# Kernel tuning notes

Measured on AMD Instinct MI355X. Metric: run time of the kernel, lower is better.

Reference implementation:

```python
import jax, jax.numpy as jnp
import numpy as np

H = 256  # hidden_size


def setup_inputs() -> dict:
    key = jax.random.key(0)
    ks = jax.random.split(key, 9)
    std = 1.0 / np.sqrt(H)
    u = lambda k, shape: jax.random.uniform(k, shape, jnp.float32, -std, std)
    x = jax.random.normal(ks[0], (64, 16, 128, 64), jnp.float32)
    return {
        "x": x,
        "wi0": u(ks[1], (64, 3 * H)),
        "wh0": u(ks[2], (H, 3 * H)),
        "bi0": u(ks[3], (3 * H,)),
        "bh0": u(ks[4], (3 * H,)),
        "wi1": u(ks[5], (H, 3 * H)),
        "wh1": u(ks[6], (H, 3 * H)),
        "bi1": u(ks[7], (3 * H,)),
        "bh1": u(ks[8], (3 * H,)),
    }


def _cell(x_t, h, wi, wh, bi, bh):
    # x_t: (B, N, D), h: (B, N, H). Gates concatenated as [r|z|n].
    gi = x_t @ wi + bi           # (B, N, 3H)
    gh = h @ wh + bh             # (B, N, 3H)
    ir, iz, inn = jnp.split(gi, 3, axis=-1)
    hr, hz, hn = jnp.split(gh, 3, axis=-1)
    r = jax.nn.sigmoid(ir + hr)
    z = jax.nn.sigmoid(iz + hz)
    n = jnp.tanh(inn + r * hn)
    return (1.0 - z) * n + z * h


def reference(x, wi0, wh0, bi0, bh0, wi1, wh1, bi1, bh1):
    seq_len, B, N, _ = x.shape
    h0 = jnp.zeros((B, N, H), x.dtype)
    h1 = jnp.zeros((B, N, H), x.dtype)

    def step(carry, x_t):
        h0, h1 = carry
        h0 = _cell(x_t, h0, wi0, wh0, bi0, bh0)
        h1 = _cell(h0, h1, wi1, wh1, bi1, bh1)
        return (h0, h1), h1

    (h0, h1), output = jax.lax.scan(step, (h0, h1), x)
    hidden_out = jnp.stack([h0, h1], axis=0)  # (num_layers, B, N, H)
    return output, hidden_out
```

## Files before the change

### kernel.cpp

```cpp
#include <hip/hip_runtime.h>


typedef __attribute__((ext_vector_type(8))) __bf16 bf8;
typedef __attribute__((ext_vector_type(8))) unsigned short u16x8;
typedef __attribute__((ext_vector_type(4))) float f32x4;

#define MFMA16(A, B, C) __builtin_amdgcn_mfma_f32_16x16x32_bf16((A), (B), (C), 0, 0, 0)

#define ROWS 2048
#define HID 256
#define NW 768
#define SLOT (ROWS * HID)
#define OUT_HID_OFF ((size_t)64 * ROWS * HID)
#define R0SLOT 524288

static __device__ __forceinline__ float b2f(unsigned short u) {
  union { unsigned u32; float f; } v;
  v.u32 = ((unsigned)u) << 16;
  return v.f;
}
static __device__ __forceinline__ unsigned short f2b(float f) {
  unsigned u = __float_as_uint(f);
  u += 0x7fffu + ((u >> 16) & 1u);
  return (unsigned short)(u >> 16);
}
static __device__ __forceinline__ float sigm(float x) {
  return 1.0f / (1.0f + __expf(-x));
}
static __device__ __forceinline__ float tanh_fast(float x) {
  x = fminf(15.0f, fmaxf(-15.0f, x));
  float e = __expf(2.0f * x);
  return (e - 1.0f) / (e + 1.0f);
}
static __device__ __forceinline__ float ldin(const void* p, int i, int f32w) {
  return f32w ? ((const float*)p)[i] : b2f(((const unsigned short*)p)[i]);
}
static __device__ __forceinline__ void stout(void* p, size_t i, float v, int f32w) {
  if (f32w) ((float*)p)[i] = v;
  else ((unsigned short*)p)[i] = f2b(v);
}

static __device__ __forceinline__ u16x8 ld_h16(const unsigned short* p) {
  union { unsigned long long q[2]; u16x8 b; } u;
  u.q[0] = __hip_atomic_load((const unsigned long long*)p, __ATOMIC_RELAXED,
                             __HIP_MEMORY_SCOPE_AGENT);
  u.q[1] = __hip_atomic_load((const unsigned long long*)(p + 4), __ATOMIC_RELAXED,
                             __HIP_MEMORY_SCOPE_AGENT);
  return u.b;
}
static __device__ __forceinline__ void st_h16(unsigned short* p, u16x8 v) {
  union { u16x8 s; unsigned long long q[2]; } u;
  u.s = v;
  __hip_atomic_store((unsigned long long*)p, u.q[0], __ATOMIC_RELAXED,
                     __HIP_MEMORY_SCOPE_AGENT);
  __hip_atomic_store((unsigned long long*)(p + 4), u.q[1], __ATOMIC_RELAXED,
                     __HIP_MEMORY_SCOPE_AGENT);
}

__global__ void probe_dtype(const unsigned short* x, unsigned* flag) {
  if (blockIdx.x != 0 || threadIdx.x != 0) return;
  int cnt = 0;
  for (int i = 0; i < 256; ++i) {
    float v = b2f(x[i]);
    if (v == v && fabsf(v) <= 8.0f) cnt++;
  }
  *flag = (cnt >= 250) ? 0u : 1u;
}

__global__ void pack_w(const void* __restrict__ W,
                       unsigned short* __restrict__ P, int KK,
                       const unsigned* __restrict__ flag) {
  int i = blockIdx.x * blockDim.x + threadIdx.x;
  int total = 48 * KK * 64;
  if (i >= total) return;
  int f32w = (int)*flag;
  int l = i & 63;
  int kk = (i >> 6) % KK;
  int nb = i / (64 * KK);
  int n = nb * 16 + (l & 15);
  int k0 = kk * 32 + (l >> 4) * 8;
  u16x8 tmp;
#pragma unroll
  for (int e = 0; e < 8; ++e) tmp[e] = f2b(ldin(W, (k0 + e) * NW + n, f32w));
  *(u16x8*)(P + (size_t)i * 8) = tmp;
}

__global__ void __launch_bounds__(256, 1) gru_main(
    const void* __restrict__ x,
    const void* __restrict__ bi0, const void* __restrict__ bh0,
    const void* __restrict__ bi1, const void* __restrict__ bh1,
    const unsigned short* __restrict__ pwi0, const unsigned short* __restrict__ pwh0,
    const unsigned short* __restrict__ pwi1, const unsigned short* __restrict__ pwh1,
    void* __restrict__ out,
    unsigned short* __restrict__ ring0, unsigned short* __restrict__ ring1,
    unsigned* __restrict__ flags, const unsigned* __restrict__ flag) {
  __shared__ __align__(16) unsigned short AS[16384];
  __shared__ __align__(16) unsigned short HS[2][2304];

  const int f32w = (int)*flag;
  const int tid = threadIdx.x;
  const int lane = tid & 63;
  const int wid = tid >> 6;
  const int bid = blockIdx.x;
  const int g = bid >> 2;
  const int slice = bid & 3;
  const int nb = slice * 4 + wid;

  const int d = nb * 16 + (lane & 15);
  const int rb = g * 32;
  const int arow = rb + (lane & 15);
  const int koff = (lane >> 4) * 8;
  const int rl = (lane >> 4) * 4;
  const int cl = wid * 16 + (lane & 15);

  unsigned* flagp = flags + (size_t)g * 64;

  const unsigned short* xw  = pwi0 + (size_t)nb * 1024;
  const unsigned short* w0  = pwh0 + (size_t)nb * 4096;
  const unsigned short* w1i = pwi1 + (size_t)nb * 4096;
  const unsigned short* w1h = pwh1 + (size_t)nb * 4096;

  const float iR0 = ldin(bi0, d, f32w) + ldin(bh0, d, f32w);
  const float iZ0 = ldin(bi0, 256 + d, f32w) + ldin(bh0, 256 + d, f32w);
  const float iI0 = ldin(bi0, 512 + d, f32w);
  const float iH0 = ldin(bh0, 512 + d, f32w);
  const float iR1 = ldin(bi1, d, f32w) + ldin(bh1, d, f32w);
  const float iZ1 = ldin(bi1, 256 + d, f32w) + ldin(bh1, 256 + d, f32w);
  const float iI1 = ldin(bi1, 512 + d, f32w);
  const float iH1 = ldin(bh1, 512 + d, f32w);

  float h0p[2][4] = {{0, 0, 0, 0}, {0, 0, 0, 0}};
  float h1p[2][4] = {{0, 0, 0, 0}, {0, 0, 0, 0}};

  const int ef = tid >> 7;
  const int ekk = (tid >> 6) & 1;
  const int eln = tid & 63;
  const int ehs = (ef * 16 + (eln & 15)) * 72 + ekk * 32 + (eln >> 4) * 8;
  const size_t ero = (size_t)g * 8192 +
                     (size_t)(ef * 8 + slice * 2 + ekk) * 512 + eln * 8;

  for (int t = 0; t <= 64; ++t) {
    const int sc = t & 1;
    const int sp = sc ^ 1;

    f32x4 aR0[2], aZ0[2], aI0[2], aH0[2], aR1[2], aZ1[2], aI1[2], aH1[2];
#pragma unroll
    for (int f = 0; f < 2; ++f) {
      aR0[f] = (f32x4){iR0, iR0, iR0, iR0};
      aZ0[f] = (f32x4){iZ0, iZ0, iZ0, iZ0};
      aI0[f] = (f32x4){iI0, iI0, iI0, iI0};
      aH0[f] = (f32x4){iH0, iH0, iH0, iH0};
      aR1[f] = (f32x4){iR1, iR1, iR1, iR1};
      aZ1[f] = (f32x4){iZ1, iZ1, iZ1, iZ1};
      aI1[f] = (f32x4){iI1, iI1, iI1, iI1};
      aH1[f] = (f32x4){iH1, iH1, iH1, iH1};
    }

    if (t < 64) {
      size_t xoff = ((size_t)t * ROWS + arow) * 64 + koff;
#pragma unroll
      for (int kk = 0; kk < 2; ++kk) {
        union { u16x8 u; bf8 b; } A0, A1;
        if (f32w) {
          const float* ab = (const float*)x + xoff;
#pragma unroll
          for (int e = 0; e < 8; ++e) {
            A0.u[e] = f2b(ab[kk * 32 + e]);
            A1.u[e] = f2b(ab[16 * 64 + kk * 32 + e]);
          }
        } else {
          const unsigned short* ab = (const unsigned short*)x + xoff;
          A0.u = *(const u16x8*)(ab + kk * 32);
          A1.u = *(const u16x8*)(ab + 16 * 64 + kk * 32);
        }
        const int lb = lane * 8;
        bf8 Br = *(const bf8*)(xw + 0 * 16384 + kk * 512 + lb);
        bf8 Bz = *(const bf8*)(xw + 1 * 16384 + kk * 512 + lb);
        bf8 Bn = *(const bf8*)(xw + 2 * 16384 + kk * 512 + lb);
        aR0[0] = MFMA16(A0.b, Br, aR0[0]);
        aR0[1] = MFMA16(A1.b, Br, aR0[1]);
        aZ0[0] = MFMA16(A0.b, Bz, aZ0[0]);
        aZ0[1] = MFMA16(A1.b, Bz, aZ0[1]);
        aI0[0] = MFMA16(A0.b, Bn, aI0[0]);
        aI0[1] = MFMA16(A1.b, Bn, aI0[1]);
      }
    }

    if (t > 0 && tid == 0) {
      const unsigned tgt = 4u * (unsigned)t;
      while (__hip_atomic_load(flagp, __ATOMIC_RELAXED,
                               __HIP_MEMORY_SCOPE_AGENT) < tgt)
        __builtin_amdgcn_s_sleep(1);
    }
    __syncthreads();

    {
      const unsigned short* r0 = ring0 + (size_t)sp * R0SLOT + (size_t)g * 8192;
#pragma unroll
      for (int i = 0; i < 4; ++i) {
        int idx = tid + i * 256;
        int ff = idx >> 6, ln2 = idx & 63;
        *(u16x8*)(AS + ff * 512 + ln2 * 8) = ld_h16(r0 + ff * 512 + ln2 * 8);
      }
      if (t >= 2) {
        const unsigned short* r1 = ring1 + (size_t)sc * R0SLOT + (size_t)g * 8192;
#pragma unroll
        for (int i = 0; i < 4; ++i) {
          int idx = tid + i * 256;
          int ff = idx >> 6, ln2 = idx & 63;
          *(u16x8*)(AS + 8192 + ff * 512 + ln2 * 8) =
              ld_h16(r1 + ff * 512 + ln2 * 8);
        }
      }
    }
    __syncthreads();

#pragma unroll
    for (int kk = 0; kk < 8; ++kk) {
      const int lb = lane * 8;
      bf8 A0 = *(const bf8*)(AS + (0 * 8 + kk) * 512 + lb);
      bf8 A1 = *(const bf8*)(AS + (1 * 8 + kk) * 512 + lb);
      bf8 Br0 = *(const bf8*)(w0 + 0 * 65536 + kk * 512 + lb);
      bf8 Bz0 = *(const bf8*)(w0 + 1 * 65536 + kk * 512 + lb);
      bf8 Bn0 = *(const bf8*)(w0 + 2 * 65536 + kk * 512 + lb);
      bf8 Br1 = *(const bf8*)(w1i + 0 * 65536 + kk * 512 + lb);
      bf8 Bz1 = *(const bf8*)(w1i + 1 * 65536 + kk * 512 + lb);
      bf8 Bn1 = *(const bf8*)(w1i + 2 * 65536 + kk * 512 + lb);
      aR0[0] = MFMA16(A0, Br0, aR0[0]);
      aR0[1] = MFMA16(A1, Br0, aR0[1]);
      aZ0[0] = MFMA16(A0, Bz0, aZ0[0]);
      aZ0[1] = MFMA16(A1, Bz0, aZ0[1]);
      aH0[0] = MFMA16(A0, Bn0, aH0[0]);
      aH0[1] = MFMA16(A1, Bn0, aH0[1]);
      aR1[0] = MFMA16(A0, Br1, aR1[0]);
      aR1[1] = MFMA16(A1, Br1, aR1[1]);
      aZ1[0] = MFMA16(A0, Bz1, aZ1[0]);
      aZ1[1] = MFMA16(A1, Bz1, aZ1[1]);
      aI1[0] = MFMA16(A0, Bn1, aI1[0]);
      aI1[1] = MFMA16(A1, Bn1, aI1[1]);
    }
    if (t >= 2) {
#pragma unroll
      for (int kk = 0; kk < 8; ++kk) {
        const int lb = lane * 8;
        bf8 A0 = *(const bf8*)(AS + 8192 + (0 * 8 + kk) * 512 + lb);
        bf8 A1 = *(const bf8*)(AS + 8192 + (1 * 8 + kk) * 512 + lb);
        bf8 Br = *(const bf8*)(w1h + 0 * 65536 + kk * 512 + lb);
        bf8 Bz = *(const bf8*)(w1h + 1 * 65536 + kk * 512 + lb);
        bf8 Bn = *(const bf8*)(w1h + 2 * 65536 + kk * 512 + lb);
        aR1[0] = MFMA16(A0, Br, aR1[0]);
        aR1[1] = MFMA16(A1, Br, aR1[1]);
        aZ1[0] = MFMA16(A0, Bz, aZ1[0]);
        aZ1[1] = MFMA16(A1, Bz, aZ1[1]);
        aH1[0] = MFMA16(A0, Bn, aH1[0]);
        aH1[1] = MFMA16(A1, Bn, aH1[1]);
      }
    }

    if (t < 64) {
#pragma unroll
      for (int f = 0; f < 2; ++f) {
#pragma unroll
        for (int j = 0; j < 4; ++j) {
          float r = sigm(aR0[f][j]);
          float z = sigm(aZ0[f][j]);
          float n = tanh_fast(aI0[f][j] + r * aH0[f][j]);
          float hv = (1.0f - z) * n + z * h0p[f][j];
          h0p[f][j] = hv;
          HS[0][(f * 16 + rl + j) * 72 + cl] = f2b(hv);
        }
      }
    }
    if (t >= 1) {
#pragma unroll
      for (int f = 0; f < 2; ++f) {
#pragma unroll
        for (int j = 0; j < 4; ++j) {
          float r = sigm(aR1[f][j]);
          float z = sigm(aZ1[f][j]);
          float n = tanh_fast(aI1[f][j] + r * aH1[f][j]);
          float hv = (1.0f - z) * n + z * h1p[f][j];
          h1p[f][j] = hv;
          HS[1][(f * 16 + rl + j) * 72 + cl] = f2b(hv);
        }
      }
    }
    __syncthreads();

    if (t < 64) {
      st_h16(ring0 + (size_t)sc * R0SLOT + ero, *(const u16x8*)(&HS[0][ehs]));
      if (t >= 1)
        st_h16(ring1 + (size_t)sp * R0SLOT + ero, *(const u16x8*)(&HS[1][ehs]));
    }

    asm volatile("s_waitcnt vmcnt(0)" ::: "memory");
    __syncthreads();
    if (t < 64 && tid == 0)
      __hip_atomic_fetch_add(flagp, 1u, __ATOMIC_RELAXED,
                             __HIP_MEMORY_SCOPE_AGENT);

    if (t >= 1) {
      const int tm1 = t - 1;
#pragma unroll
      for (int f = 0; f < 2; ++f) {
#pragma unroll
        for (int j = 0; j < 4; ++j) {
          int row = rb + f * 16 + rl + j;
          stout(out, ((size_t)tm1 * ROWS + row) * HID + d, h1p[f][j], f32w);
          if (tm1 == 63)
            stout(out, OUT_HID_OFF + (size_t)SLOT + (size_t)row * HID + d,
                  h1p[f][j], f32w);
        }
      }
    }
    if (t == 63) {
#pragma unroll
      for (int f = 0; f < 2; ++f) {
#pragma unroll
        for (int j = 0; j < 4; ++j) {
          int row = rb + f * 16 + rl + j;
          stout(out, OUT_HID_OFF + (size_t)row * HID + d, h0p[f][j], f32w);
        }
      }
    }
  }
}

extern "C" void kernel_launch(void* const* d_in, const int* in_sizes, int n_in,
                              void* d_out, int out_size, void* d_ws, size_t ws_size,
                              hipStream_t stream) {
  (void)in_sizes; (void)n_in; (void)out_size; (void)ws_size;
  const void* x   = d_in[0];
  const void* wi0 = d_in[1];
  const void* wh0 = d_in[2];
  const void* bi0 = d_in[3];
  const void* bh0 = d_in[4];
  const void* wi1 = d_in[5];
  const void* wh1 = d_in[6];
  const void* bi1 = d_in[7];
  const void* bh1 = d_in[8];
  void* out = d_out;

  char* ws = (char*)d_ws;
  unsigned* flags = (unsigned*)ws;
  unsigned* flag  = (unsigned*)(ws + 16384);
  unsigned short* ring0 = (unsigned short*)(ws + 32768);
  unsigned short* ring1 = (unsigned short*)(ws + 32768 + 2097152);
  unsigned short* pwi0 = (unsigned short*)(ws + 32768 + 4194304);
  unsigned short* pwh0 = pwi0 + 49152;
  unsigned short* pwi1 = pwh0 + 196608;
  unsigned short* pwh1 = pwi1 + 196608;

  hipMemsetAsync(d_ws, 0, 32768 + 2097152, stream);

  probe_dtype<<<1, 64, 0, stream>>>((const unsigned short*)x, flag);

  pack_w<<<(48 * 2 * 64 + 255) / 256, 256, 0, stream>>>(wi0, pwi0, 2, flag);
  pack_w<<<(48 * 8 * 64 + 255) / 256, 256, 0, stream>>>(wh0, pwh0, 8, flag);
  pack_w<<<(48 * 8 * 64 + 255) / 256, 256, 0, stream>>>(wi1, pwi1, 8, flag);
  pack_w<<<(48 * 8 * 64 + 255) / 256, 256, 0, stream>>>(wh1, pwh1, 8, flag);

  void* kargs[] = {&x, &bi0, &bh0, &bi1, &bh1, &pwi0, &pwh0, &pwi1, &pwh1,
                   &out, &ring0, &ring1, &flags, &flag};
  hipError_t lerr = hipLaunchCooperativeKernel(
      (const void*)gru_main, dim3(256), dim3(256), kargs, 0, stream);
  if (lerr != hipSuccess) {
    (void)hipGetLastError();
    gru_main<<<dim3(256), dim3(256), 0, stream>>>(
        x, bi0, bh0, bi1, bh1, pwi0, pwh0, pwi1, pwh1,
        out, ring0, ring1, flags, flag);
  }
}
```

Measured before the change: 733.2 us.

## Halve row groups, split layer flags, keep layer-0 weights in registers

```diff
diff --git a/kernel.cpp b/kernel.cpp
--- a/kernel.cpp
+++ b/kernel.cpp
@@ -12,7 +12,7 @@
 #define NW 768
 #define SLOT (ROWS * HID)
 #define OUT_HID_OFF ((size_t)64 * ROWS * HID)
-#define R0SLOT 524288
+#define RSLOT 524288
 
 static __device__ __forceinline__ float b2f(unsigned short u) {
   union { unsigned u32; float f; } v;
@@ -85,7 +85,7 @@
   *(u16x8*)(P + (size_t)i * 8) = tmp;
 }
 
-__global__ void __launch_bounds__(256, 1) gru_main(
+__global__ void __launch_bounds__(256, 2) gru_main(
     const void* __restrict__ x,
     const void* __restrict__ bi0, const void* __restrict__ bh0,
     const void* __restrict__ bi1, const void* __restrict__ bh1,
@@ -94,8 +94,8 @@
     void* __restrict__ out,
     unsigned short* __restrict__ ring0, unsigned short* __restrict__ ring1,
     unsigned* __restrict__ flags, const unsigned* __restrict__ flag) {
-  __shared__ __align__(16) unsigned short AS[16384];
-  __shared__ __align__(16) unsigned short HS[2][2304];
+  __shared__ __align__(16) unsigned short AS[8192];
+  __shared__ __align__(16) unsigned short HS[2][1152];
 
   const int f32w = (int)*flag;
   const int tid = threadIdx.x;
@@ -107,18 +107,31 @@
   const int nb = slice * 4 + wid;
 
   const int d = nb * 16 + (lane & 15);
-  const int rb = g * 32;
+  const int rb = g * 16;
   const int arow = rb + (lane & 15);
   const int koff = (lane >> 4) * 8;
   const int rl = (lane >> 4) * 4;
-  const int cl = wid * 16 + (lane & 15);
-
-  unsigned* flagp = flags + (size_t)g * 64;
+
+  unsigned* flag0p = flags + (size_t)g * 64;
+  unsigned* flag1p = flag0p + 32;
 
   const unsigned short* xw  = pwi0 + (size_t)nb * 1024;
   const unsigned short* w0  = pwh0 + (size_t)nb * 4096;
   const unsigned short* w1i = pwi1 + (size_t)nb * 4096;
   const unsigned short* w1h = pwh1 + (size_t)nb * 4096;
+
+  bf8 w0r[3][8];
+#pragma unroll
+  for (int gate = 0; gate < 3; ++gate)
+#pragma unroll
+    for (int kk = 0; kk < 8; ++kk)
+      w0r[gate][kk] = *(const bf8*)(w0 + gate * 65536 + kk * 512 + lane * 8);
+  bf8 wxr[3][2];
+#pragma unroll
+  for (int gate = 0; gate < 3; ++gate)
+#pragma unroll
+    for (int kk = 0; kk < 2; ++kk)
+      wxr[gate][kk] = *(const bf8*)(xw + gate * 16384 + kk * 512 + lane * 8);
 
   const float iR0 = ldin(bi0, d, f32w) + ldin(bh0, d, f32w);
   const float iZ0 = ldin(bi0, 256 + d, f32w) + ldin(bh0, 256 + d, f32w);
@@ -129,198 +142,163 @@
   const float iI1 = ldin(bi1, 512 + d, f32w);
   const float iH1 = ldin(bh1, 512 + d, f32w);
 
-  float h0p[2][4] = {{0, 0, 0, 0}, {0, 0, 0, 0}};
-  float h1p[2][4] = {{0, 0, 0, 0}, {0, 0, 0, 0}};
-
-  const int ef = tid >> 7;
+  float h0p[4] = {0, 0, 0, 0};
+  float h1p[4] = {0, 0, 0, 0};
+
   const int ekk = (tid >> 6) & 1;
   const int eln = tid & 63;
-  const int ehs = (ef * 16 + (eln & 15)) * 72 + ekk * 32 + (eln >> 4) * 8;
-  const size_t ero = (size_t)g * 8192 +
-                     (size_t)(ef * 8 + slice * 2 + ekk) * 512 + eln * 8;
+  const int ehs = (eln & 15) * 72 + ekk * 32 + (eln >> 4) * 8;
+  const size_t ero = (size_t)g * 4096 + (size_t)(slice * 2 + ekk) * 512 + eln * 8;
 
   for (int t = 0; t <= 64; ++t) {
     const int sc = t & 1;
     const int sp = sc ^ 1;
 
-    f32x4 aR0[2], aZ0[2], aI0[2], aH0[2], aR1[2], aZ1[2], aI1[2], aH1[2];
-#pragma unroll
-    for (int f = 0; f < 2; ++f) {
-      aR0[f] = (f32x4){iR0, iR0, iR0, iR0};
-      aZ0[f] = (f32x4){iZ0, iZ0, iZ0, iZ0};
-      aI0[f] = (f32x4){iI0, iI0, iI0, iI0};
-      aH0[f] = (f32x4){iH0, iH0, iH0, iH0};
-      aR1[f] = (f32x4){iR1, iR1, iR1, iR1};
-      aZ1[f] = (f32x4){iZ1, iZ1, iZ1, iZ1};
-      aI1[f] = (f32x4){iI1, iI1, iI1, iI1};
-      aH1[f] = (f32x4){iH1, iH1, iH1, iH1};
-    }
+    f32x4 aR0 = {iR0, iR0, iR0, iR0}, aZ0 = {iZ0, iZ0, iZ0, iZ0};
+    f32x4 aI0 = {iI0, iI0, iI0, iI0}, aH0 = {iH0, iH0, iH0, iH0};
+    f32x4 aR1 = {iR1, iR1, iR1, iR1}, aZ1 = {iZ1, iZ1, iZ1, iZ1};
+    f32x4 aI1 = {iI1, iI1, iI1, iI1}, aH1 = {iH1, iH1, iH1, iH1};
 
     if (t < 64) {
       size_t xoff = ((size_t)t * ROWS + arow) * 64 + koff;
 #pragma unroll
       for (int kk = 0; kk < 2; ++kk) {
-        union { u16x8 u; bf8 b; } A0, A1;
+        union { u16x8 u; bf8 b; } A0;
         if (f32w) {
           const float* ab = (const float*)x + xoff;
 #pragma unroll
-          for (int e = 0; e < 8; ++e) {
-            A0.u[e] = f2b(ab[kk * 32 + e]);
-            A1.u[e] = f2b(ab[16 * 64 + kk * 32 + e]);
-          }
+          for (int e = 0; e < 8; ++e) A0.u[e] = f2b(ab[kk * 32 + e]);
         } else {
-          const unsigned short* ab = (const unsigned short*)x + xoff;
-          A0.u = *(const u16x8*)(ab + kk * 32);
-          A1.u = *(const u16x8*)(ab + 16 * 64 + kk * 32);
+          A0.u = *(const u16x8*)((const unsigned short*)x + xoff + kk * 32);
         }
-        const int lb = lane * 8;
-        bf8 Br = *(const bf8*)(xw + 0 * 16384 + kk * 512 + lb);
-        bf8 Bz = *(const bf8*)(xw + 1 * 16384 + kk * 512 + lb);
-        bf8 Bn = *(const bf8*)(xw + 2 * 16384 + kk * 512 + lb);
-        aR0[0] = MFMA16(A0.b, Br, aR0[0]);
-        aR0[1] = MFMA16(A1.b, Br, aR0[1]);
-        aZ0[0] = MFMA16(A0.b, Bz, aZ0[0]);
-        aZ0[1] = MFMA16(A1.b, Bz, aZ0[1]);
-        aI0[0] = MFMA16(A0.b, Bn, aI0[0]);
-        aI0[1] = MFMA16(A1.b, Bn, aI0[1]);
-      }
-    }
-
-    if (t > 0 && tid == 0) {
-      const unsigned tgt = 4u * (unsigned)t;
-      while (__hip_atomic_load(flagp, __ATOMIC_RELAXED,
-                               __HIP_MEMORY_SCOPE_AGENT) < tgt)
-        __builtin_amdgcn_s_sleep(1);
+        aR0 = MFMA16(A0.b, wxr[0][kk], aR0);
+        aZ0 = MFMA16(A0.b, wxr[1][kk], aZ0);
+        aI0 = MFMA16(A0.b, wxr[2][kk], aI0);
+      }
+    }
+
+    if (tid == 0) {
+      if (t >= 2) {
+        const unsigned tgt = 4u * (unsigned)(t - 1);
+        while (__hip_atomic_load(flag1p, __ATOMIC_RELAXED,
+                                 __HIP_MEMORY_SCOPE_AGENT) < tgt)
+          __builtin_amdgcn_s_sleep(1);
+      }
+      if (t >= 1) {
+        const unsigned tgt = 4u * (unsigned)t;
+        while (__hip_atomic_load(flag0p, __ATOMIC_RELAXED,
+                                 __HIP_MEMORY_SCOPE_AGENT) < tgt)
+          __builtin_amdgcn_s_sleep(1);
+      }
     }
     __syncthreads();
 
-    {
-      const unsigned short* r0 = ring0 + (size_t)sp * R0SLOT + (size_t)g * 8192;
-#pragma unroll
-      for (int i = 0; i < 4; ++i) {
+    if (t >= 1) {
+      const unsigned short* r0 = ring0 + (size_t)sp * RSLOT + (size_t)g * 4096;
+#pragma unroll
+      for (int i = 0; i < 2; ++i) {
         int idx = tid + i * 256;
         int ff = idx >> 6, ln2 = idx & 63;
         *(u16x8*)(AS + ff * 512 + ln2 * 8) = ld_h16(r0 + ff * 512 + ln2 * 8);
       }
-      if (t >= 2) {
-        const unsigned short* r1 = ring1 + (size_t)sc * R0SLOT + (size_t)g * 8192;
-#pragma unroll
-        for (int i = 0; i < 4; ++i) {
-          int idx = tid + i * 256;
-          int ff = idx >> 6, ln2 = idx & 63;
-          *(u16x8*)(AS + 8192 + ff * 512 + ln2 * 8) =
-              ld_h16(r1 + ff * 512 + ln2 * 8);
+    }
+    if (t >= 2) {
+      const unsigned short* r1 = ring1 + (size_t)sc * RSLOT + (size_t)g * 4096;
+#pragma unroll
+      for (int i = 0; i < 2; ++i) {
+        int idx = tid + i * 256;
+        int ff = idx >> 6, ln2 = idx & 63;
+        *(u16x8*)(AS + 4096 + ff * 512 + ln2 * 8) =
+            ld_h16(r1 + ff * 512 + ln2 * 8);
+      }
+    }
+    __syncthreads();
+
+    if (t < 64) {
+      if (t >= 1) {
+#pragma unroll
+        for (int kk = 0; kk < 8; ++kk) {
+          bf8 A = *(const bf8*)(AS + kk * 512 + lane * 8);
+          aR0 = MFMA16(A, w0r[0][kk], aR0);
+          aZ0 = MFMA16(A, w0r[1][kk], aZ0);
+          aH0 = MFMA16(A, w0r[2][kk], aH0);
         }
       }
+#pragma unroll
+      for (int j = 0; j < 4; ++j) {
+        float r = sigm(aR0[j]);
+        float z = sigm(aZ0[j]);
+        float n = tanh_fast(aI0[j] + r * aH0[j]);
+        float hv = (1.0f - z) * n + z * h0p[j];
+        h0p[j] = hv;
+        HS[0][(rl + j) * 72 + wid * 16 + (lane & 15)] = f2b(hv);
+      }
     }
     __syncthreads();
 
-#pragma unroll
-    for (int kk = 0; kk < 8; ++kk) {
-      const int lb = lane * 8;
-      bf8 A0 = *(const bf8*)(AS + (0 * 8 + kk) * 512 + lb);
-      bf8 A1 = *(const bf8*)(AS + (1 * 8 + kk) * 512 + lb);
-      bf8 Br0 = *(const bf8*)(w0 + 0 * 65536 + kk * 512 + lb);
-      bf8 Bz0 = *(const bf8*)(w0 + 1 * 65536 + kk * 512 + lb);
-      bf8 Bn0 = *(const bf8*)(w0 + 2 * 65536 + kk * 512 + lb);
-      bf8 Br1 = *(const bf8*)(w1i + 0 * 65536 + kk * 512 + lb);
-      bf8 Bz1 = *(const bf8*)(w1i + 1 * 65536 + kk * 512 + lb);
-      bf8 Bn1 = *(const bf8*)(w1i + 2 * 65536 + kk * 512 + lb);
-      aR0[0] = MFMA16(A0, Br0, aR0[0]);
-      aR0[1] = MFMA16(A1, Br0, aR0[1]);
-      aZ0[0] = MFMA16(A0, Bz0, aZ0[0]);
-      aZ0[1] = MFMA16(A1, Bz0, aZ0[1]);
-      aH0[0] = MFMA16(A0, Bn0, aH0[0]);
-      aH0[1] = MFMA16(A1, Bn0, aH0[1]);
-      aR1[0] = MFMA16(A0, Br1, aR1[0]);
-      aR1[1] = MFMA16(A1, Br1, aR1[1]);
-      aZ1[0] = MFMA16(A0, Bz1, aZ1[0]);
-      aZ1[1] = MFMA16(A1, Bz1, aZ1[1]);
-      aI1[0] = MFMA16(A0, Bn1, aI1[0]);
-      aI1[1] = MFMA16(A1, Bn1, aI1[1]);
-    }
-    if (t >= 2) {
+    if (t < 64 && tid < 128)
+      st_h16(ring0 + (size_t)sc * RSLOT + ero, *(const u16x8*)(&HS[0][ehs]));
+    asm volatile("s_waitcnt vmcnt(0)" ::: "memory");
+    if (t < 64 && tid == 0)
+      __hip_atomic_fetch_add(flag0p, 1u, __ATOMIC_RELAXED,
+                             __HIP_MEMORY_SCOPE_AGENT);
+
+    if (t >= 1) {
 #pragma unroll
       for (int kk = 0; kk < 8; ++kk) {
         const int lb = lane * 8;
-        bf8 A0 = *(const bf8*)(AS + 8192 + (0 * 8 + kk) * 512 + lb);
-        bf8 A1 = *(const bf8*)(AS + 8192 + (1 * 8 + kk) * 512 + lb);
-        bf8 Br = *(const bf8*)(w1h + 0 * 65536 + kk * 512 + lb);
-        bf8 Bz = *(const bf8*)(w1h + 1 * 65536 + kk * 512 + lb);
-        bf8 Bn = *(const bf8*)(w1h + 2 * 65536 + kk * 512 + lb);
-        aR1[0] = MFMA16(A0, Br, aR1[0]);
-        aR1[1] = MFMA16(A1, Br, aR1[1]);
-        aZ1[0] = MFMA16(A0, Bz, aZ1[0]);
-        aZ1[1] = MFMA16(A1, Bz, aZ1[1]);
-        aH1[0] = MFMA16(A0, Bn, aH1[0]);
-        aH1[1] = MFMA16(A1, Bn, aH1[1]);
-      }
-    }
-
-    if (t < 64) {
-#pragma unroll
-      for (int f = 0; f < 2; ++f) {
-#pragma unroll
-        for (int j = 0; j < 4; ++j) {
-          float r = sigm(aR0[f][j]);
-          float z = sigm(aZ0[f][j]);
-          float n = tanh_fast(aI0[f][j] + r * aH0[f][j]);
-          float hv = (1.0f - z) * n + z * h0p[f][j];
-          h0p[f][j] = hv;
-          HS[0][(f * 16 + rl + j) * 72 + cl] = f2b(hv);
+        bf8 A0 = *(const bf8*)(AS + kk * 512 + lb);
+        bf8 Br1 = *(const bf8*)(w1i + 0 * 65536 + kk * 512 + lb);
+        bf8 Bz1 = *(const bf8*)(w1i + 1 * 65536 + kk * 512 + lb);
+        bf8 Bn1 = *(const bf8*)(w1i + 2 * 65536 + kk * 512 + lb);
+        aR1 = MFMA16(A0, Br1, aR1);
+        aZ1 = MFMA16(A0, Bz1, aZ1);
+        aI1 = MFMA16(A0, Bn1, aI1);
+        if (t >= 2) {
+          bf8 A1 = *(const bf8*)(AS + 4096 + kk * 512 + lb);
+          bf8 Br = *(const bf8*)(w1h + 0 * 65536 + kk * 512 + lb);
+          bf8 Bz = *(const bf8*)(w1h + 1 * 65536 + kk * 512 + lb);
+          bf8 Bn = *(const bf8*)(w1h + 2 * 65536 + kk * 512 + lb);
+          aR1 = MFMA16(A1, Br, aR1);
+          aZ1 = MFMA16(A1, Bz, aZ1);
+          aH1 = MFMA16(A1, Bn, aH1);
         }
       }
-    }
-    if (t >= 1) {
-#pragma unroll
-      for (int f = 0; f < 2; ++f) {
-#pragma unroll
-        for (int j = 0; j < 4; ++j) {
-          float r = sigm(aR1[f][j]);
-          float z = sigm(aZ1[f][j]);
-          float n = tanh_fast(aI1[f][j] + r * aH1[f][j]);
-          float hv = (1.0f - z) * n + z * h1p[f][j];
-          h1p[f][j] = hv;
-          HS[1][(f * 16 + rl + j) * 72 + cl] = f2b(hv);
-        }
+#pragma unroll
+      for (int j = 0; j < 4; ++j) {
+        float r = sigm(aR1[j]);
+        float z = sigm(aZ1[j]);
+        float n = tanh_fast(aI1[j] + r * aH1[j]);
+        float hv = (1.0f - z) * n + z * h1p[j];
+        h1p[j] = hv;
+        HS[1][(rl + j) * 72 + wid * 16 + (lane & 15)] = f2b(hv);
       }
     }
     __syncthreads();
 
-    if (t < 64) {
-      st_h16(ring0 + (size_t)sc * R0SLOT + ero, *(const u16x8*)(&HS[0][ehs]));
-      if (t >= 1)
-        st_h16(ring1 + (size_t)sp * R0SLOT + ero, *(const u16x8*)(&HS[1][ehs]));
-    }
-
+    if (t >= 1 && t < 64 && tid < 128)
+      st_h16(ring1 + (size_t)sp * RSLOT + ero, *(const u16x8*)(&HS[1][ehs]));
     asm volatile("s_waitcnt vmcnt(0)" ::: "memory");
-    __syncthreads();
-    if (t < 64 && tid == 0)
-      __hip_atomic_fetch_add(flagp, 1u, __ATOMIC_RELAXED,
+    if (t >= 1 && t < 64 && tid == 0)
+      __hip_atomic_fetch_add(flag1p, 1u, __ATOMIC_RELAXED,
                              __HIP_MEMORY_SCOPE_AGENT);
 
     if (t >= 1) {
       const int tm1 = t - 1;
 #pragma unroll
-      for (int f = 0; f < 2; ++f) {
-#pragma unroll
-        for (int j = 0; j < 4; ++j) {
-          int row = rb + f * 16 + rl + j;
-          stout(out, ((size_t)tm1 * ROWS + row) * HID + d, h1p[f][j], f32w);
-          if (tm1 == 63)
-            stout(out, OUT_HID_OFF + (size_t)SLOT + (size_t)row * HID + d,
-                  h1p[f][j], f32w);
-        }
+      for (int j = 0; j < 4; ++j) {
+        int row = rb + rl + j;
+        stout(out, ((size_t)tm1 * ROWS + row) * HID + d, h1p[j], f32w);
+        if (tm1 == 63)
+          stout(out, OUT_HID_OFF + (size_t)SLOT + (size_t)row * HID + d,
+                h1p[j], f32w);
       }
     }
     if (t == 63) {
 #pragma unroll
-      for (int f = 0; f < 2; ++f) {
-#pragma unroll
-        for (int j = 0; j < 4; ++j) {
-          int row = rb + f * 16 + rl + j;
-          stout(out, OUT_HID_OFF + (size_t)row * HID + d, h0p[f][j], f32w);
-        }
+      for (int j = 0; j < 4; ++j) {
+        int row = rb + rl + j;
+        stout(out, OUT_HID_OFF + (size_t)row * HID + d, h0p[j], f32w);
       }
     }
   }
@@ -343,15 +321,15 @@
 
   char* ws = (char*)d_ws;
   unsigned* flags = (unsigned*)ws;
-  unsigned* flag  = (unsigned*)(ws + 16384);
-  unsigned short* ring0 = (unsigned short*)(ws + 32768);
-  unsigned short* ring1 = (unsigned short*)(ws + 32768 + 2097152);
-  unsigned short* pwi0 = (unsigned short*)(ws + 32768 + 4194304);
+  unsigned* flag  = (unsigned*)(ws + 32768);
+  unsigned short* ring0 = (unsigned short*)(ws + 36864);
+  unsigned short* ring1 = (unsigned short*)(ws + 36864 + 2097152);
+  unsigned short* pwi0 = (unsigned short*)(ws + 36864 + 4194304);
   unsigned short* pwh0 = pwi0 + 49152;
   unsigned short* pwi1 = pwh0 + 196608;
   unsigned short* pwh1 = pwi1 + 196608;
 
-  hipMemsetAsync(d_ws, 0, 32768 + 2097152, stream);
+  hipMemsetAsync(d_ws, 0, 36864, stream);
 
   probe_dtype<<<1, 64, 0, stream>>>((const unsigned short*)x, flag);
 
@@ -363,10 +341,10 @@
   void* kargs[] = {&x, &bi0, &bh0, &bi1, &bh1, &pwi0, &pwh0, &pwi1, &pwh1,
                    &out, &ring0, &ring1, &flags, &flag};
   hipError_t lerr = hipLaunchCooperativeKernel(
-      (const void*)gru_main, dim3(256), dim3(256), kargs, 0, stream);
+      (const void*)gru_main, dim3(512), dim3(256), kargs, 0, stream);
   if (lerr != hipSuccess) {
     (void)hipGetLastError();
-    gru_main<<<dim3(256), dim3(256), 0, stream>>>(
+    gru_main<<<dim3(512), dim3(256), 0, stream>>>(
         x, bi0, bh0, bi1, bh1, pwi0, pwh0, pwi1, pwh1,
         out, ring0, ring1, flags, flag);
   }
```

Measured after the change: 1.514 ms. 106% more time.
